# Kernel optimization log

Measured on AMD Instinct MI355X. Metric: run time of the kernel, lower is better.

Reference implementation:

```python
import jax, jax.numpy as jnp
import numpy as np

N_NODES = 50000
N_EDGES = 800000
N_GRAPHS = 512
F_IN = 9
U = 64  # model_units


def _add_self_loops(edge_index, n):
    loop = jnp.arange(n, dtype=edge_index.dtype)
    return jnp.concatenate([edge_index, jnp.stack([loop, loop])], axis=1)


def gat_conv(x, edge_index, W, a_src, a_dst, b):
    # PyG GATConv, heads=1, negative_slope=0.2, add_self_loops=True
    n = x.shape[0]
    ei = _add_self_loops(edge_index, n)
    src, dst = ei[0], ei[1]
    h = x @ W                              # [n, U]
    alpha_s = h @ a_src                    # [n]
    alpha_d = h @ a_dst                    # [n]
    e = jax.nn.leaky_relu(alpha_s[src] + alpha_d[dst], 0.2)   # [E+n]
    m = jax.ops.segment_max(e, dst, num_segments=n)           # stable softmax over incoming edges
    ex = jnp.exp(e - m[dst])
    denom = jax.ops.segment_sum(ex, dst, num_segments=n)
    coef = ex / denom[dst]                 # [E+n]
    out = jax.ops.segment_sum(h[src] * coef[:, None], dst, num_segments=n)
    return out + b


def gcn_conv(x, edge_index, W, b):
    # PyG GCNConv with symmetric normalization and self loops
    n = x.shape[0]
    ei = _add_self_loops(edge_index, n)
    src, dst = ei[0], ei[1]
    h = x @ W                              # [n, U]
    deg = jax.ops.segment_sum(jnp.ones(src.shape, h.dtype), dst, num_segments=n)
    dinv = jnp.where(deg > 0, jax.lax.rsqrt(deg), 0.0)
    norm = dinv[src] * dinv[dst]           # [E+n]
    out = jax.ops.segment_sum(h[src] * norm[:, None], dst, num_segments=n)
    return out + b


def _branch(x, edge_index, W_gat, a_src, a_dst, b_gat, W_gcn, b_gcn, W1, b1, W2, b2, W3, b3):
    x = jnp.tanh(gat_conv(x, edge_index, W_gat, a_src, a_dst, b_gat))
    for i in range(W_gcn.shape[0]):        # model_layers - 1 = 2 GCN layers
        x = jnp.tanh(gcn_conv(x, edge_index, W_gcn[i], b_gcn[i]))
        # dropout is a no-op in eval mode
    x = jnp.tanh(x @ W1 + b1)
    x = jnp.tanh(x @ W2 + b2)
    x = x @ W3 + b3                        # [n, 1]; dropout no-op in eval
    return x


def _mean_pool(x, batch, num_graphs):
    sums = jax.ops.segment_sum(x, batch, num_segments=num_graphs)
    cnt = jax.ops.segment_sum(jnp.ones((x.shape[0],), x.dtype), batch, num_segments=num_graphs)
    return sums / jnp.maximum(cnt, 1.0)[:, None]


def setup_inputs() -> dict:
    key = jax.random.key(0)
    ks = jax.random.split(key, 16)
    inp = {
        "x_a": jax.random.normal(ks[0], (N_NODES, F_IN), jnp.float32),
        "x_b": jax.random.normal(ks[1], (N_NODES, F_IN), jnp.float32),
        "edge_index_a": jax.random.randint(ks[2], (2, N_EDGES), 0, N_NODES, jnp.int32),
        "edge_index_b": jax.random.randint(ks[3], (2, N_EDGES), 0, N_NODES, jnp.int32),
        "batch_a": jnp.sort(jax.random.randint(ks[4], (N_NODES,), 0, N_GRAPHS, jnp.int32)),
        "batch_b": jnp.sort(jax.random.randint(ks[5], (N_NODES,), 0, N_GRAPHS, jnp.int32)),
        # parameters
        "W_gat": jax.random.normal(ks[6], (F_IN, U), jnp.float32) * 0.3,
        "a_src": jax.random.normal(ks[7], (U,), jnp.float32) * 0.3,
        "a_dst": jax.random.normal(ks[8], (U,), jnp.float32) * 0.3,
        "b_gat": jnp.zeros((U,), jnp.float32),
        "W_gcn": jax.random.normal(ks[9], (2, U, U), jnp.float32) * (1.0 / np.sqrt(U)),
        "b_gcn": jnp.zeros((2, U), jnp.float32),
        "W1": jax.random.normal(ks[10], (U, U), jnp.float32) * (1.0 / np.sqrt(U)),
        "b1": jnp.zeros((U,), jnp.float32),
        "W2": jax.random.normal(ks[11], (U, 32), jnp.float32) * (1.0 / np.sqrt(U)),
        "b2": jnp.zeros((32,), jnp.float32),
        "W3": jax.random.normal(ks[12], (32, 1), jnp.float32) * (1.0 / np.sqrt(32.0)),
        "b3": jnp.zeros((1,), jnp.float32),
    }
    return inp


def reference(x_a, x_b, edge_index_a, edge_index_b, batch_a, batch_b,
              W_gat, a_src, a_dst, b_gat, W_gcn, b_gcn, W1, b1, W2, b2, W3, b3):
    params = (W_gat, a_src, a_dst, b_gat, W_gcn, b_gcn, W1, b1, W2, b2, W3, b3)
    ha = _branch(x_a, edge_index_a, *params)
    hb = _branch(x_b, edge_index_b, *params)
    ua = _mean_pool(ha, batch_a, N_GRAPHS)   # [G, 1]
    ub = _mean_pool(hb, batch_b, N_GRAPHS)
    return jax.nn.sigmoid(ub - ua)
```

## Files before the change

### kernel.cpp

```cpp
#include <hip/hip_runtime.h>
#include <hip/hip_fp16.h>
#include <math.h>

#define NN 50000
#define NE 800000
#define NG 512
#define NET (NE + NN)
#define NT2 ((2 * NN + 63) / 64)
#define GN4 ((2 * NN + 3) / 4)
#define GN8 ((2 * NN + 7) / 8)
#define GN32 ((2 * NN + 31) / 32)
#define TS 72

#define SLICE 512
#define NSL ((NN + SLICE - 1) / SLICE)
#define CHK 4096
#define NCK ((NET + CHK - 1) / CHK)
#define CAP 10240

typedef unsigned short u16;
typedef _Float16 h8 __attribute__((ext_vector_type(8)));
typedef float f32x4 __attribute__((ext_vector_type(4)));

__device__ __forceinline__ float wsum64(float v) {
#pragma unroll
    for (int o = 32; o > 0; o >>= 1) v += __shfl_down(v, o, 64);
    return v;
}

__device__ __forceinline__ float fast_tanh(float x) {
    return 1.f - 2.f / (__expf(2.f * x) + 1.f);
}


__global__ __launch_bounds__(256) void k_hist(const int* __restrict__ eia,
                                              const int* __restrict__ eib,
                                              int* __restrict__ cnts) {
    __shared__ int h[NSL];
    int b = blockIdx.x;
    int br = b >= NCK, c = b - (br ? NCK : 0);
    int t = threadIdx.x;
    for (int i = t; i < NSL; i += 256) h[i] = 0;
    __syncthreads();
    const int* ei = br ? eib : eia;
    int e0 = c * CHK, e1 = e0 + CHK; if (e1 > NET) e1 = NET;
    for (int e = e0 + t; e < e1; e += 256) {
        int d = (e < NE) ? __builtin_nontemporal_load(&ei[NE + e]) : (e - NE);
        atomicAdd(&h[d >> 9], 1);
    }
    __syncthreads();
    for (int i = t; i < NSL; i += 256) cnts[(br * NSL + i) * NCK + c] = h[i];
}

__global__ __launch_bounds__(64) void k_off1(int* __restrict__ cnts,
                                             int* __restrict__ sliceBase) {
    int b = blockIdx.x;
    int br = b >= NSL, s = b - (br ? NSL : 0);
    int lane = threadIdx.x;
    int* row = cnts + (br * NSL + s) * NCK;
    int run = 0;
    for (int c0 = 0; c0 < NCK; c0 += 64) {
        int c = c0 + lane;
        int v = (c < NCK) ? row[c] : 0;
        int orig = v;
#pragma unroll
        for (int o = 1; o < 64; o <<= 1) {
            int tv = __shfl_up(v, o, 64);
            if (lane >= o) v += tv;
        }
        if (c < NCK) row[c] = run + v - orig;
        run += __shfl(v, 63, 64);
    }
    if (lane == 0) sliceBase[br * (NSL + 1) + s] = run;
}

__global__ void k_off2(int* __restrict__ sliceBase, int* __restrict__ rowptr2,
                       float* __restrict__ pool) {
    int t = threadIdx.x;
    for (int i = t; i < 4 * NG; i += 256) pool[i] = 0.f;
    if (t < 2) {
        int* sb = sliceBase + t * (NSL + 1);
        int run = 0;
        for (int s = 0; s < NSL; s++) { int v = sb[s]; sb[s] = run; run += v; }
        sb[NSL] = run;
        rowptr2[t * (NN + 1) + NN] = run;
    }
}

__global__ __launch_bounds__(256) void k_bucket(const int* __restrict__ eia,
                                                const int* __restrict__ eib,
                                                const int* __restrict__ cnts,
                                                const int* __restrict__ sliceBase,
                                                unsigned int* __restrict__ staging) {
    __shared__ int cur[NSL];
    int b = blockIdx.x;
    int br = b >= NCK, c = b - (br ? NCK : 0);
    int t = threadIdx.x;
    for (int i = t; i < NSL; i += 256)
        cur[i] = cnts[(br * NSL + i) * NCK + c] + sliceBase[br * (NSL + 1) + i];
    __syncthreads();
    const int* ei = br ? eib : eia;
    unsigned int* stg = staging + (size_t)br * NET;
    int e0 = c * CHK, e1 = e0 + CHK; if (e1 > NET) e1 = NET;
    for (int e = e0 + t; e < e1; e += 256) {
        int d, s;
        if (e < NE) {
            d = __builtin_nontemporal_load(&ei[NE + e]);
            s = __builtin_nontemporal_load(&ei[e]);
        } else { d = e - NE; s = d; }
        int pos = atomicAdd(&cur[d >> 9], 1);
        stg[pos] = ((unsigned int)(d & 511) << 16) | (unsigned int)s;
    }
}

__global__ __launch_bounds__(512) void k_slice(const unsigned int* __restrict__ staging,
                                               const int* __restrict__ sliceBase,
                                               int* __restrict__ rowptr2,
                                               float* __restrict__ dinv2,
                                               u16* __restrict__ csr2) {
    __shared__ int sc[512];
    __shared__ int cur[512];
    __shared__ u16 buf[CAP];
    int b = blockIdx.x;
    int br = b >= NSL, sl = b - (br ? NSL : 0);
    int t = threadIdx.x;
    const int* sb = sliceBase + br * (NSL + 1);
    int base = sb[sl], m = sb[sl + 1] - base;
    const unsigned int* st = staging + (size_t)br * NET + base;
    cur[t] = 0;
    __syncthreads();
    for (int i = t; i < m; i += 512) atomicAdd(&cur[st[i] >> 16], 1);
    __syncthreads();
    int v = cur[t];
    sc[t] = v;
    __syncthreads();
    for (int o = 1; o < 512; o <<= 1) {
        int add = (t >= o) ? sc[t - o] : 0;
        __syncthreads();
        sc[t] += add;
        __syncthreads();
    }
    int excl = sc[t] - v;
    int node = sl * SLICE + t;
    if (node < NN) {
        rowptr2[br * (NN + 1) + node] = base + excl;
        dinv2[br * NN + node] = v > 0 ? rsqrtf((float)v) : 0.f;
    }
    cur[t] = excl;
    __syncthreads();
    for (int i = t; i < m; i += 512) {
        unsigned int e = st[i];
        int pos = atomicAdd(&cur[e >> 16], 1);
        if (pos < CAP) buf[pos] = (u16)(e & 0xffffu);
    }
    __syncthreads();
    u16* out = csr2 + (size_t)br * NET + base;
    int mm = m < CAP ? m : CAP;
    for (int i = t; i < mm; i += 512) out[i] = buf[i];
}

__global__ __launch_bounds__(256) void k_wprep(const float* __restrict__ W1,
                                               const float* __restrict__ W2,
                                               const float* __restrict__ Wgcn,
                                               __half* __restrict__ out) {
    int i = blockIdx.x * 256 + threadIdx.x;
    float v;
    if (i < 4096)       { int n = i >> 6,        k = i & 63; v = W1[k * 64 + n]; }
    else if (i < 6144)  { int j = i - 4096; int n = j >> 6, k = j & 63; v = W2[k * 32 + n]; }
    else if (i < 10240) { int j = i - 6144; int n = j >> 6, k = j & 63; v = Wgcn[k * 64 + n]; }
    else                { int j = i - 10240; int n = j >> 6, k = j & 63; v = Wgcn[4096 + k * 64 + n]; }
    out[i] = __float2half(v);
}


__global__ void k_gat_input(const float* __restrict__ xa, const float* __restrict__ xb,
                            const float* __restrict__ Wg,
                            const float* __restrict__ avs, const float* __restrict__ avd,
                            __half* __restrict__ A, float* __restrict__ als,
                            float* __restrict__ ald) {
    __shared__ float sW[9 * 64];
    __shared__ float sas[64], sad[64];
    int t = threadIdx.x;
    for (int i = t; i < 9 * 64; i += 256) sW[i] = Wg[i];
    if (t < 64) { sas[t] = avs[t]; sad[t] = avd[t]; }
    __syncthreads();
    int n = blockIdx.x * 4 + (t >> 6);
    int u = t & 63;
    if (n >= 2 * NN) return;
    const float* xp = (n < NN) ? &xa[(size_t)n * 9] : &xb[(size_t)(n - NN) * 9];
    float h = 0.f;
#pragma unroll
    for (int f = 0; f < 9; f++) h += xp[f] * sW[f * 64 + u];
    A[(size_t)n * 64 + u] = __float2half(h);
    float ps = wsum64(h * sas[u]);
    float pd = wsum64(h * sad[u]);
    if (u == 0) { als[n] = ps; ald[n] = pd; }
}

__global__ __launch_bounds__(256) void k_edgew(
        const int* __restrict__ rowptr2, const u16* __restrict__ csr2,
        const float* __restrict__ als, const float* __restrict__ ald,
        float* __restrict__ wn) {
    int u = threadIdx.x & 63;
    int lu = u & 31;
    int dg = blockIdx.x * 8 + (threadIdx.x >> 6) * 2 + (u >> 5);
    if (dg >= 2 * NN) return;
    int br = dg >= NN;
    int d = dg - br * NN;
    const int* rp = rowptr2 + br * (NN + 1);
    const u16* cs = csr2 + br * NET;
    float* wp = wn + (size_t)br * NET;
    int nb = br * NN;
    int beg = rp[d], end = rp[d + 1];
    float ad = ald[dg];
    float den = 0.f;
    for (int c = beg + lu; c < end; c += 32) {
        int s = nb + cs[c];
        float v = als[s] + ad;
        float w = __expf(fmaxf(v, 0.2f * v));
        den += w;
        wp[c] = w;
    }
#pragma unroll
    for (int o = 16; o > 0; o >>= 1) den += __shfl_down(den, o, 32);
    den = __shfl(den, 0, 32);
    float inv = 1.f / den;
    for (int c = beg + lu; c < end; c += 32) wp[c] *= inv;
}

__device__ __forceinline__ void fma8(float* acc, float4 f, float w) {
    const __half2* h = (const __half2*)&f;
#pragma unroll
    for (int p = 0; p < 4; p++) {
        float2 v = __half22float2(h[p]);
        acc[2 * p]     += v.x * w;
        acc[2 * p + 1] += v.y * w;
    }
}

__global__ __launch_bounds__(256) void k_gat_gather8(
        const int* __restrict__ rowptr2, const u16* __restrict__ csr2,
        const float* __restrict__ wn, const __half* __restrict__ A,
        const float* __restrict__ bias, __half* __restrict__ B) {
    int lane = threadIdx.x & 63;
    int grp = lane >> 3, li = lane & 7;
    int dg = blockIdx.x * 32 + (threadIdx.x >> 6) * 8 + grp;
    int br = dg >= NN;
    int d = dg - br * NN;
    const int* rp = rowptr2 + br * (NN + 1);
    const u16* cs = csr2 + br * NET;
    const float* wp = wn + (size_t)br * NET;
    int nb = br * NN;
    int beg = rp[d], end = rp[d + 1];
    const float4* Af = (const float4*)A;
    float acc[8];
#pragma unroll
    for (int k = 0; k < 8; k++) acc[k] = 0.f;
    for (int j = beg; j < end; j += 4) {
        int i0 = j, i1 = j + 1, i2 = j + 2, i3 = j + 3;
        int c1 = i1 < end ? i1 : end - 1;
        int c2 = i2 < end ? i2 : end - 1;
        int c3 = i3 < end ? i3 : end - 1;
        float w0 = wp[i0];
        float w1 = i1 < end ? wp[c1] : 0.f;
        float w2 = i2 < end ? wp[c2] : 0.f;
        float w3 = i3 < end ? wp[c3] : 0.f;
        int s0 = nb + cs[i0];
        int s1 = nb + cs[c1];
        int s2 = nb + cs[c2];
        int s3 = nb + cs[c3];
        float4 f0 = Af[(size_t)s0 * 8 + li];
        float4 f1 = Af[(size_t)s1 * 8 + li];
        float4 f2 = Af[(size_t)s2 * 8 + li];
        float4 f3 = Af[(size_t)s3 * 8 + li];
        fma8(acc, f0, w0);
        fma8(acc, f1, w1);
        fma8(acc, f2, w2);
        fma8(acc, f3, w3);
    }
    const float4* bf = (const float4*)bias;
    float4 b0 = bf[2 * li], b1 = bf[2 * li + 1];
    __half2 o[4];
    o[0] = __floats2half2_rn(fast_tanh(acc[0] + b0.x), fast_tanh(acc[1] + b0.y));
    o[1] = __floats2half2_rn(fast_tanh(acc[2] + b0.z), fast_tanh(acc[3] + b0.w));
    o[2] = __floats2half2_rn(fast_tanh(acc[4] + b1.x), fast_tanh(acc[5] + b1.y));
    o[3] = __floats2half2_rn(fast_tanh(acc[6] + b1.z), fast_tanh(acc[7] + b1.w));
    ((float4*)B)[(size_t)dg * 8 + li] = *(float4*)o;
}

__global__ __launch_bounds__(256) void k_gcn_gather8(
        const int* __restrict__ rowptr2, const u16* __restrict__ csr2,
        const float* __restrict__ dinv, const __half* __restrict__ Y,
        const float* __restrict__ bias, __half* __restrict__ Bout) {
    int lane = threadIdx.x & 63;
    int grp = lane >> 3, li = lane & 7;
    int dg = blockIdx.x * 32 + (threadIdx.x >> 6) * 8 + grp;
    int br = dg >= NN;
    int d = dg - br * NN;
    const int* rp = rowptr2 + br * (NN + 1);
    const u16* cs = csr2 + br * NET;
    int nb = br * NN;
    int beg = rp[d], end = rp[d + 1];
    const float4* Yf = (const float4*)Y;
    float acc[8];
#pragma unroll
    for (int k = 0; k < 8; k++) acc[k] = 0.f;
    for (int j = beg; j < end; j += 4) {
        int i1 = j + 1, i2 = j + 2, i3 = j + 3;
        int c1 = i1 < end ? i1 : end - 1;
        int c2 = i2 < end ? i2 : end - 1;
        int c3 = i3 < end ? i3 : end - 1;
        float w1 = i1 < end ? 1.f : 0.f;
        float w2 = i2 < end ? 1.f : 0.f;
        float w3 = i3 < end ? 1.f : 0.f;
        int s0 = nb + cs[j];
        int s1 = nb + cs[c1];
        int s2 = nb + cs[c2];
        int s3 = nb + cs[c3];
        float4 f0 = Yf[(size_t)s0 * 8 + li];
        float4 f1 = Yf[(size_t)s1 * 8 + li];
        float4 f2 = Yf[(size_t)s2 * 8 + li];
        float4 f3 = Yf[(size_t)s3 * 8 + li];
        fma8(acc, f0, 1.f);
        fma8(acc, f1, w1);
        fma8(acc, f2, w2);
        fma8(acc, f3, w3);
    }
    float dv = dinv[dg];
    const float4* bf = (const float4*)bias;
    float4 b0 = bf[2 * li], b1 = bf[2 * li + 1];
    __half2 o[4];
    o[0] = __floats2half2_rn(fast_tanh(acc[0] * dv + b0.x), fast_tanh(acc[1] * dv + b0.y));
    o[1] = __floats2half2_rn(fast_tanh(acc[2] * dv + b0.z), fast_tanh(acc[3] * dv + b0.w));
    o[2] = __floats2half2_rn(fast_tanh(acc[4] * dv + b1.x), fast_tanh(acc[5] * dv + b1.y));
    o[3] = __floats2half2_rn(fast_tanh(acc[6] * dv + b1.z), fast_tanh(acc[7] * dv + b1.w));
    ((float4*)Bout)[(size_t)dg * 8 + li] = *(float4*)o;
}

__global__ __launch_bounds__(256) void k_lin_tile(
        const __half* __restrict__ X, const __half* __restrict__ Wt,
        const float* __restrict__ dinv, __half* __restrict__ Y) {
    __shared__ __half sX[64 * TS];
    __shared__ __half sW[64 * TS];
    int t = threadIdx.x;
    int base = blockIdx.x * 64;
    const float4* Xf = (const float4*)X;
    const float4* Wf = (const float4*)Wt;
#pragma unroll
    for (int rep = 0; rep < 2; rep++) {
        int i = t + rep * 256;
        int row = i >> 3, q = i & 7;
        *(float4*)&sW[row * TS + q * 8] = Wf[i];
        float4 x;
        if (base + row < 2 * NN) x = Xf[(size_t)(base + row) * 8 + q];
        else x = make_float4(0.f, 0.f, 0.f, 0.f);
        *(float4*)&sX[row * TS + q * 8] = x;
    }
    __syncthreads();
    int l = t & 63, w = t >> 6;
    int lr = l & 15, lg = l >> 4;
    h8 av0 = *(const h8*)&sX[(16 * w + lr) * TS + 8 * lg];
    h8 av1 = *(const h8*)&sX[(16 * w + lr) * TS + 32 + 8 * lg];
    f32x4 acc[4];
#pragma unroll
    for (int s = 0; s < 4; s++) {
        h8 bv0 = *(const h8*)&sW[(16 * s + lr) * TS + 8 * lg];
        h8 bv1 = *(const h8*)&sW[(16 * s + lr) * TS + 32 + 8 * lg];
        f32x4 c = {0.f, 0.f, 0.f, 0.f};
        c = __builtin_amdgcn_mfma_f32_16x16x32_f16(av0, bv0, c, 0, 0, 0);
        c = __builtin_amdgcn_mfma_f32_16x16x32_f16(av1, bv1, c, 0, 0, 0);
        acc[s] = c;
    }
    int nrow = base + 16 * w + 4 * lg;
    float4 dv4 = *(const float4*)&dinv[16 * w + 4 * lg + base];
#pragma unroll
    for (int s = 0; s < 4; s++) {
        int col = 16 * s + lr;
#pragma unroll
        for (int i = 0; i < 4; i++) {
            int n = nrow + i;
            if (n < 2 * NN) Y[(size_t)n * 64 + col] = __float2half(acc[s][i] * dv4[i]);
        }
    }
}

__global__ __launch_bounds__(256) void k_mlp_pool(
        const __half* __restrict__ X,
        const int* __restrict__ batch_a, const int* __restrict__ batch_b,
        const __half* __restrict__ W1t, const float* __restrict__ b1,
        const __half* __restrict__ W2t, const float* __restrict__ b2,
        const float* __restrict__ W3, const float* __restrict__ b3,
        float* __restrict__ pool) {
    __shared__ __half sX[64 * TS];
    __shared__ __half sW1[64 * TS];
    __shared__ __half sW2[32 * TS];
    __shared__ float sP[64];
    __shared__ int sKey[64];
    __shared__ float sVal[64];
    int t = threadIdx.x;
    int base = blockIdx.x * 64;
    const float4* Xf = (const float4*)X;
    const float4* W1f = (const float4*)W1t;
    const float4* W2f = (const float4*)W2t;
#pragma unroll
    for (int rep = 0; rep < 2; rep++) {
        int i = t + rep * 256;
        int row = i >> 3, q = i & 7;
        *(float4*)&sW1[row * TS + q * 8] = W1f[i];
        float4 x;
        if (base + row < 2 * NN) x = Xf[(size_t)(base + row) * 8 + q];
        else x = make_float4(0.f, 0.f, 0.f, 0.f);
        *(float4*)&sX[row * TS + q * 8] = x;
    }
    {
        int row = t >> 3, q = t & 7;
        *(float4*)&sW2[row * TS + q * 8] = W2f[t];
    }
    float bb3 = b3[0];
    __syncthreads();
    int l = t & 63, w = t >> 6;
    int lr = l & 15, lg = l >> 4;
    h8 av0 = *(const h8*)&sX[(16 * w + lr) * TS + 8 * lg];
    h8 av1 = *(const h8*)&sX[(16 * w + lr) * TS + 32 + 8 * lg];
    f32x4 d1[4];
#pragma unroll
    for (int s = 0; s < 4; s++) {
        float bias = b1[16 * s + lr];
        f32x4 c = {bias, bias, bias, bias};
        h8 bv0 = *(const h8*)&sW1[(16 * s + lr) * TS + 8 * lg];
        h8 bv1 = *(const h8*)&sW1[(16 * s + lr) * TS + 32 + 8 * lg];
        c = __builtin_amdgcn_mfma_f32_16x16x32_f16(av0, bv0, c, 0, 0, 0);
        c = __builtin_amdgcn_mfma_f32_16x16x32_f16(av1, bv1, c, 0, 0, 0);
        d1[s] = c;
    }
#pragma unroll
    for (int s = 0; s < 4; s++) {
#pragma unroll
        for (int i = 0; i < 4; i++) {
            sX[(16 * w + 4 * lg + i) * TS + 16 * s + lr] = __float2half(fast_tanh(d1[s][i]));
        }
    }
    __syncthreads();
    h8 a20 = *(const h8*)&sX[(16 * w + lr) * TS + 8 * lg];
    h8 a21 = *(const h8*)&sX[(16 * w + lr) * TS + 32 + 8 * lg];
    f32x4 d2[2];
#pragma unroll
    for (int s = 0; s < 2; s++) {
        float bias = b2[16 * s + lr];
        f32x4 c = {bias, bias, bias, bias};
        h8 bv0 = *(const h8*)&sW2[(16 * s + lr) * TS + 8 * lg];
        h8 bv1 = *(const h8*)&sW2[(16 * s + lr) * TS + 32 + 8 * lg];
        c = __builtin_amdgcn_mfma_f32_16x16x32_f16(a20, bv0, c, 0, 0, 0);
        c = __builtin_amdgcn_mfma_f32_16x16x32_f16(a21, bv1, c, 0, 0, 0);
        d2[s] = c;
    }
    float w3a = W3[lr], w3b = W3[16 + lr];
    float pr[4];
#pragma unroll
    for (int i = 0; i < 4; i++)
        pr[i] = fast_tanh(d2[0][i]) * w3a + fast_tanh(d2[1][i]) * w3b;
#pragma unroll
    for (int o = 1; o < 16; o <<= 1) {
#pragma unroll
        for (int i = 0; i < 4; i++) pr[i] += __shfl_xor(pr[i], o, 16);
    }
    if (lr == 0) {
#pragma unroll
        for (int i = 0; i < 4; i++) sP[16 * w + 4 * lg + i] = pr[i];
    }
    __syncthreads();
    if (t < 64) {
        int n = base + t;
        bool valid = n < 2 * NN;
        int br = n >= NN;
        int g = valid ? (br ? batch_b[n - NN] : batch_a[n]) : -1;
        int key = valid ? (br * 4096 + g) : -1;
        sKey[t] = key;
        sVal[t] = sP[t] + bb3;
        __builtin_amdgcn_s_barrier();
        if (valid && (t == 0 || sKey[t - 1] != key)) {
            float sum = 0.f;
            int cnt = 0;
            for (int j = t; j < 64 && sKey[j] == key; j++) { sum += sVal[j]; cnt++; }
            float* bin = pool + br * 2 * NG;
            atomicAdd(&bin[g], sum);
            atomicAdd(&bin[NG + g], (float)cnt);
        }
    }
}

__global__ void k_final(const float* __restrict__ pool, float* __restrict__ out) {
    int g = blockIdx.x * 256 + threadIdx.x;
    if (g >= NG) return;
    float ua = pool[g] / fmaxf(pool[NG + g], 1.f);
    float ub = pool[2 * NG + g] / fmaxf(pool[3 * NG + g], 1.f);
    float z = ub - ua;
    out[g] = 1.f / (1.f + __expf(-z));
}

extern "C" void kernel_launch(void* const* d_in, const int* in_sizes, int n_in,
                              void* d_out, int out_size, void* d_ws, size_t ws_size,
                              hipStream_t stream) {
    const float* x_a = (const float*)d_in[0];
    const float* x_b = (const float*)d_in[1];
    const int* ei_a = (const int*)d_in[2];
    const int* ei_b = (const int*)d_in[3];
    const int* batch_a = (const int*)d_in[4];
    const int* batch_b = (const int*)d_in[5];
    const float* Wg   = (const float*)d_in[6];
    const float* avs  = (const float*)d_in[7];
    const float* avd  = (const float*)d_in[8];
    const float* bg   = (const float*)d_in[9];
    const float* Wgcn = (const float*)d_in[10];
    const float* bgcn = (const float*)d_in[11];
    const float* W1 = (const float*)d_in[12];
    const float* b1 = (const float*)d_in[13];
    const float* W2 = (const float*)d_in[14];
    const float* b2 = (const float*)d_in[15];
    const float* W3 = (const float*)d_in[16];
    const float* b3 = (const float*)d_in[17];

    char* w = (char*)d_ws;
    __half* A2 = (__half*)w;          w += (size_t)2 * NN * 64 * 2;
    __half* B2 = (__half*)w;          w += (size_t)2 * NN * 64 * 2;
    float* als2 = (float*)w;          w += (size_t)2 * NN * 4;
    float* ald2 = (float*)w;          w += (size_t)2 * NN * 4;
    float* dinv2 = (float*)w;         w += (size_t)2 * NN * 4;
    float* pool = (float*)w;          w += (size_t)4 * NG * 4;
    int* rowptr2 = (int*)w;           w += (size_t)2 * (NN + 1) * 4;
    int* cnts = (int*)w;              w += (size_t)2 * NSL * NCK * 4;
    int* sliceBase = (int*)w;         w += (size_t)2 * (NSL + 1) * 4;
    u16* csr2 = (u16*)w;              w += (size_t)2 * NET * 2;
    float* wn = (float*)w;            w += (size_t)2 * NET * 4;
    __half* wcache = (__half*)w;      w += (size_t)14336 * 2;
    unsigned int* staging = (unsigned int*)A2;

    __half* W1t = wcache;
    __half* W2t = wcache + 4096;
    __half* Wg0t = wcache + 6144;
    __half* Wg1t = wcache + 10240;

    dim3 blk(256);

    k_hist<<<2 * NCK, blk, 0, stream>>>(ei_a, ei_b, cnts);
    k_wprep<<<56, blk, 0, stream>>>(W1, W2, Wgcn, wcache);
    k_off1<<<2 * NSL, dim3(64), 0, stream>>>(cnts, sliceBase);
    k_off2<<<1, blk, 0, stream>>>(sliceBase, rowptr2, pool);
    k_bucket<<<2 * NCK, blk, 0, stream>>>(ei_a, ei_b, cnts, sliceBase, staging);
    k_slice<<<2 * NSL, dim3(512), 0, stream>>>(staging, sliceBase, rowptr2, dinv2, csr2);

    k_gat_input<<<GN4, blk, 0, stream>>>(x_a, x_b, Wg, avs, avd, A2, als2, ald2);
    k_edgew<<<GN8, blk, 0, stream>>>(rowptr2, csr2, als2, ald2, wn);
    k_gat_gather8<<<GN32, blk, 0, stream>>>(rowptr2, csr2, wn, A2, bg, B2);
    k_lin_tile<<<NT2, blk, 0, stream>>>(B2, Wg0t, dinv2, A2);
    k_gcn_gather8<<<GN32, blk, 0, stream>>>(rowptr2, csr2, dinv2, A2, bgcn, B2);
    k_lin_tile<<<NT2, blk, 0, stream>>>(B2, Wg1t, dinv2, A2);
    k_gcn_gather8<<<GN32, blk, 0, stream>>>(rowptr2, csr2, dinv2, A2, bgcn + 64, B2);
    k_mlp_pool<<<NT2, blk, 0, stream>>>(B2, batch_a, batch_b, W1t, b1, W2t, b2, W3, b3, pool);

    k_final<<<(NG + 255) / 256, blk, 0, stream>>>(pool, (float*)d_out);
}
```

Measured before the change: 304.4 us.

## Split node features into 32-wide halves and fuse GAT edge weights into gather

Node feature buffers move from row-major [n,64] fp16 to two planes of [n,32], and the gather kernels process one half per block. Block IDs are interleaved so paired half-blocks run close together. The goal is a smaller random-access working set per gather pass, which should improve L2 hit rates. The separate edge-weight kernel and its wn buffer are removed: GAT weights are recomputed inside the gather, with normalization applied at the end. The cost is that exp is computed twice, once for each half, and the CSR indices are read twice.

Result: no change. 304.9 us (+0.2%).

```diff
diff --git a/kernel.cpp b/kernel.cpp
--- a/kernel.cpp
+++ b/kernel.cpp
@@ -8,9 +8,10 @@
 #define NET (NE + NN)
 #define NT2 ((2 * NN + 63) / 64)
 #define GN4 ((2 * NN + 3) / 4)
-#define GN8 ((2 * NN + 7) / 8)
-#define GN32 ((2 * NN + 31) / 32)
 #define TS 72
+#define HOFF ((size_t)2 * NN * 32)
+#define GXB 391
+#define GX (8 * GXB)
 
 #define SLICE 512
 #define NSL ((NN + SLICE - 1) / SLICE)
@@ -191,41 +192,10 @@
     float h = 0.f;
 #pragma unroll
     for (int f = 0; f < 9; f++) h += xp[f] * sW[f * 64 + u];
-    A[(size_t)n * 64 + u] = __float2half(h);
+    A[(size_t)(u >> 5) * HOFF + (size_t)n * 32 + (u & 31)] = __float2half(h);
     float ps = wsum64(h * sas[u]);
     float pd = wsum64(h * sad[u]);
     if (u == 0) { als[n] = ps; ald[n] = pd; }
-}
-
-__global__ __launch_bounds__(256) void k_edgew(
-        const int* __restrict__ rowptr2, const u16* __restrict__ csr2,
-        const float* __restrict__ als, const float* __restrict__ ald,
-        float* __restrict__ wn) {
-    int u = threadIdx.x & 63;
-    int lu = u & 31;
-    int dg = blockIdx.x * 8 + (threadIdx.x >> 6) * 2 + (u >> 5);
-    if (dg >= 2 * NN) return;
-    int br = dg >= NN;
-    int d = dg - br * NN;
-    const int* rp = rowptr2 + br * (NN + 1);
-    const u16* cs = csr2 + br * NET;
-    float* wp = wn + (size_t)br * NET;
-    int nb = br * NN;
-    int beg = rp[d], end = rp[d + 1];
-    float ad = ald[dg];
-    float den = 0.f;
-    for (int c = beg + lu; c < end; c += 32) {
-        int s = nb + cs[c];
-        float v = als[s] + ad;
-        float w = __expf(fmaxf(v, 0.2f * v));
-        den += w;
-        wp[c] = w;
-    }
-#pragma unroll
-    for (int o = 16; o > 0; o >>= 1) den += __shfl_down(den, o, 32);
-    den = __shfl(den, 0, 32);
-    float inv = 1.f / den;
-    for (int c = beg + lu; c < end; c += 32) wp[c] *= inv;
 }
 
 __device__ __forceinline__ void fma8(float* acc, float4 f, float w) {
@@ -238,73 +208,91 @@
     }
 }
 
-__global__ __launch_bounds__(256) void k_gat_gather8(
+__global__ __launch_bounds__(256) void k_gat_gather(
         const int* __restrict__ rowptr2, const u16* __restrict__ csr2,
-        const float* __restrict__ wn, const __half* __restrict__ A,
-        const float* __restrict__ bias, __half* __restrict__ B) {
-    int lane = threadIdx.x & 63;
-    int grp = lane >> 3, li = lane & 7;
-    int dg = blockIdx.x * 32 + (threadIdx.x >> 6) * 8 + grp;
-    int br = dg >= NN;
-    int d = dg - br * NN;
+        const float* __restrict__ als, const float* __restrict__ ald,
+        const __half* __restrict__ A, const float* __restrict__ bias,
+        __half* __restrict__ B) {
+    int bid = blockIdx.x;
+    int br = (bid >> 2) & 1;
+    int h = (bid >> 1) & 1;
+    int k = ((bid >> 3) << 1) + (bid & 1);
+    int t = threadIdx.x;
+    int lane = t & 63;
+    int grp = lane >> 2, li = lane & 3;
+    int d = k * 64 + ((t >> 6) << 4) + grp;
+    if (d >= NN) return;
+    int dg = br * NN + d;
     const int* rp = rowptr2 + br * (NN + 1);
     const u16* cs = csr2 + br * NET;
-    const float* wp = wn + (size_t)br * NET;
     int nb = br * NN;
     int beg = rp[d], end = rp[d + 1];
-    const float4* Af = (const float4*)A;
+    float ad = ald[dg];
+    const float4* Af = (const float4*)A + (size_t)h * 2 * NN * 4;
     float acc[8];
 #pragma unroll
-    for (int k = 0; k < 8; k++) acc[k] = 0.f;
+    for (int q = 0; q < 8; q++) acc[q] = 0.f;
+    float den = 0.f;
     for (int j = beg; j < end; j += 4) {
-        int i0 = j, i1 = j + 1, i2 = j + 2, i3 = j + 3;
+        int i1 = j + 1, i2 = j + 2, i3 = j + 3;
         int c1 = i1 < end ? i1 : end - 1;
         int c2 = i2 < end ? i2 : end - 1;
         int c3 = i3 < end ? i3 : end - 1;
-        float w0 = wp[i0];
-        float w1 = i1 < end ? wp[c1] : 0.f;
-        float w2 = i2 < end ? wp[c2] : 0.f;
-        float w3 = i3 < end ? wp[c3] : 0.f;
-        int s0 = nb + cs[i0];
+        int s0 = nb + cs[j];
         int s1 = nb + cs[c1];
         int s2 = nb + cs[c2];
         int s3 = nb + cs[c3];
-        float4 f0 = Af[(size_t)s0 * 8 + li];
-        float4 f1 = Af[(size_t)s1 * 8 + li];
-        float4 f2 = Af[(size_t)s2 * 8 + li];
-        float4 f3 = Af[(size_t)s3 * 8 + li];
+        float v0 = als[s0] + ad;
+        float v1 = als[s1] + ad;
+        float v2 = als[s2] + ad;
+        float v3 = als[s3] + ad;
+        float w0 = __expf(fmaxf(v0, 0.2f * v0));
+        float w1 = i1 < end ? __expf(fmaxf(v1, 0.2f * v1)) : 0.f;
+        float w2 = i2 < end ? __expf(fmaxf(v2, 0.2f * v2)) : 0.f;
+        float w3 = i3 < end ? __expf(fmaxf(v3, 0.2f * v3)) : 0.f;
+        den += (w0 + w1) + (w2 + w3);
+        float4 f0 = Af[(size_t)s0 * 4 + li];
+        float4 f1 = Af[(size_t)s1 * 4 + li];
+        float4 f2 = Af[(size_t)s2 * 4 + li];
+        float4 f3 = Af[(size_t)s3 * 4 + li];
         fma8(acc, f0, w0);
         fma8(acc, f1, w1);
         fma8(acc, f2, w2);
         fma8(acc, f3, w3);
     }
+    float inv = 1.f / den;
     const float4* bf = (const float4*)bias;
-    float4 b0 = bf[2 * li], b1 = bf[2 * li + 1];
+    float4 b0 = bf[h * 8 + li * 2], b1 = bf[h * 8 + li * 2 + 1];
     __half2 o[4];
-    o[0] = __floats2half2_rn(fast_tanh(acc[0] + b0.x), fast_tanh(acc[1] + b0.y));
-    o[1] = __floats2half2_rn(fast_tanh(acc[2] + b0.z), fast_tanh(acc[3] + b0.w));
-    o[2] = __floats2half2_rn(fast_tanh(acc[4] + b1.x), fast_tanh(acc[5] + b1.y));
-    o[3] = __floats2half2_rn(fast_tanh(acc[6] + b1.z), fast_tanh(acc[7] + b1.w));
-    ((float4*)B)[(size_t)dg * 8 + li] = *(float4*)o;
-}
-
-__global__ __launch_bounds__(256) void k_gcn_gather8(
+    o[0] = __floats2half2_rn(fast_tanh(acc[0] * inv + b0.x), fast_tanh(acc[1] * inv + b0.y));
+    o[1] = __floats2half2_rn(fast_tanh(acc[2] * inv + b0.z), fast_tanh(acc[3] * inv + b0.w));
+    o[2] = __floats2half2_rn(fast_tanh(acc[4] * inv + b1.x), fast_tanh(acc[5] * inv + b1.y));
+    o[3] = __floats2half2_rn(fast_tanh(acc[6] * inv + b1.z), fast_tanh(acc[7] * inv + b1.w));
+    ((float4*)B)[(size_t)h * 2 * NN * 4 + (size_t)dg * 4 + li] = *(float4*)o;
+}
+
+__global__ __launch_bounds__(256) void k_gcn_gather(
         const int* __restrict__ rowptr2, const u16* __restrict__ csr2,
         const float* __restrict__ dinv, const __half* __restrict__ Y,
         const float* __restrict__ bias, __half* __restrict__ Bout) {
-    int lane = threadIdx.x & 63;
-    int grp = lane >> 3, li = lane & 7;
-    int dg = blockIdx.x * 32 + (threadIdx.x >> 6) * 8 + grp;
-    int br = dg >= NN;
-    int d = dg - br * NN;
+    int bid = blockIdx.x;
+    int br = (bid >> 2) & 1;
+    int h = (bid >> 1) & 1;
+    int k = ((bid >> 3) << 1) + (bid & 1);
+    int t = threadIdx.x;
+    int lane = t & 63;
+    int grp = lane >> 2, li = lane & 3;
+    int d = k * 64 + ((t >> 6) << 4) + grp;
+    if (d >= NN) return;
+    int dg = br * NN + d;
     const int* rp = rowptr2 + br * (NN + 1);
     const u16* cs = csr2 + br * NET;
     int nb = br * NN;
     int beg = rp[d], end = rp[d + 1];
-    const float4* Yf = (const float4*)Y;
+    const float4* Yf = (const float4*)Y + (size_t)h * 2 * NN * 4;
     float acc[8];
 #pragma unroll
-    for (int k = 0; k < 8; k++) acc[k] = 0.f;
+    for (int q = 0; q < 8; q++) acc[q] = 0.f;
     for (int j = beg; j < end; j += 4) {
         int i1 = j + 1, i2 = j + 2, i3 = j + 3;
         int c1 = i1 < end ? i1 : end - 1;
@@ -317,10 +305,10 @@
         int s1 = nb + cs[c1];
         int s2 = nb + cs[c2];
         int s3 = nb + cs[c3];
-        float4 f0 = Yf[(size_t)s0 * 8 + li];
-        float4 f1 = Yf[(size_t)s1 * 8 + li];
-        float4 f2 = Yf[(size_t)s2 * 8 + li];
-        float4 f3 = Yf[(size_t)s3 * 8 + li];
+        float4 f0 = Yf[(size_t)s0 * 4 + li];
+        float4 f1 = Yf[(size_t)s1 * 4 + li];
+        float4 f2 = Yf[(size_t)s2 * 4 + li];
+        float4 f3 = Yf[(size_t)s3 * 4 + li];
         fma8(acc, f0, 1.f);
         fma8(acc, f1, w1);
         fma8(acc, f2, w2);
@@ -328,13 +316,28 @@
     }
     float dv = dinv[dg];
     const float4* bf = (const float4*)bias;
-    float4 b0 = bf[2 * li], b1 = bf[2 * li + 1];
+    float4 b0 = bf[h * 8 + li * 2], b1 = bf[h * 8 + li * 2 + 1];
     __half2 o[4];
     o[0] = __floats2half2_rn(fast_tanh(acc[0] * dv + b0.x), fast_tanh(acc[1] * dv + b0.y));
     o[1] = __floats2half2_rn(fast_tanh(acc[2] * dv + b0.z), fast_tanh(acc[3] * dv + b0.w));
     o[2] = __floats2half2_rn(fast_tanh(acc[4] * dv + b1.x), fast_tanh(acc[5] * dv + b1.y));
     o[3] = __floats2half2_rn(fast_tanh(acc[6] * dv + b1.z), fast_tanh(acc[7] * dv + b1.w));
-    ((float4*)Bout)[(size_t)dg * 8 + li] = *(float4*)o;
+    ((float4*)Bout)[(size_t)h * 2 * NN * 4 + (size_t)dg * 4 + li] = *(float4*)o;
+}
+
+__device__ __forceinline__ void stage_split(const __half* __restrict__ X, int base,
+                                            __half* sX, int t) {
+    const float4* Xf = (const float4*)X;
+#pragma unroll
+    for (int rep = 0; rep < 2; rep++) {
+        int i = t + rep * 256;
+        int row = i >> 3, q = i & 7;
+        int h = q >> 2, q2 = q & 3;
+        float4 x;
+        if (base + row < 2 * NN) x = Xf[(size_t)h * 2 * NN * 4 + (size_t)(base + row) * 4 + q2];
+        else x = make_float4(0.f, 0.f, 0.f, 0.f);
+        *(float4*)&sX[row * TS + q * 8] = x;
+    }
 }
 
 __global__ __launch_bounds__(256) void k_lin_tile(
@@ -344,18 +347,14 @@
     __shared__ __half sW[64 * TS];
     int t = threadIdx.x;
     int base = blockIdx.x * 64;
-    const float4* Xf = (const float4*)X;
     const float4* Wf = (const float4*)Wt;
 #pragma unroll
     for (int rep = 0; rep < 2; rep++) {
         int i = t + rep * 256;
         int row = i >> 3, q = i & 7;
         *(float4*)&sW[row * TS + q * 8] = Wf[i];
-        float4 x;
-        if (base + row < 2 * NN) x = Xf[(size_t)(base + row) * 8 + q];
-        else x = make_float4(0.f, 0.f, 0.f, 0.f);
-        *(float4*)&sX[row * TS + q * 8] = x;
-    }
+    }
+    stage_split(X, base, sX, t);
     __syncthreads();
     int l = t & 63, w = t >> 6;
     int lr = l & 15, lg = l >> 4;
@@ -376,10 +375,11 @@
 #pragma unroll
     for (int s = 0; s < 4; s++) {
         int col = 16 * s + lr;
+        size_t cbase = (size_t)(col >> 5) * HOFF + (col & 31);
 #pragma unroll
         for (int i = 0; i < 4; i++) {
             int n = nrow + i;
-            if (n < 2 * NN) Y[(size_t)n * 64 + col] = __float2half(acc[s][i] * dv4[i]);
+            if (n < 2 * NN) Y[cbase + (size_t)n * 32] = __float2half(acc[s][i] * dv4[i]);
         }
     }
 }
@@ -399,7 +399,6 @@
     __shared__ float sVal[64];
     int t = threadIdx.x;
     int base = blockIdx.x * 64;
-    const float4* Xf = (const float4*)X;
     const float4* W1f = (const float4*)W1t;
     const float4* W2f = (const float4*)W2t;
 #pragma unroll
@@ -407,15 +406,12 @@
         int i = t + rep * 256;
         int row = i >> 3, q = i & 7;
         *(float4*)&sW1[row * TS + q * 8] = W1f[i];
-        float4 x;
-        if (base + row < 2 * NN) x = Xf[(size_t)(base + row) * 8 + q];
-        else x = make_float4(0.f, 0.f, 0.f, 0.f);
-        *(float4*)&sX[row * TS + q * 8] = x;
     }
     {
         int row = t >> 3, q = t & 7;
         *(float4*)&sW2[row * TS + q * 8] = W2f[t];
     }
+    stage_split(X, base, sX, t);
     float bb3 = b3[0];
     __syncthreads();
     int l = t & 63, w = t >> 6;
@@ -531,7 +527,6 @@
     int* cnts = (int*)w;              w += (size_t)2 * NSL * NCK * 4;
     int* sliceBase = (int*)w;         w += (size_t)2 * (NSL + 1) * 4;
     u16* csr2 = (u16*)w;              w += (size_t)2 * NET * 2;
-    float* wn = (float*)w;            w += (size_t)2 * NET * 4;
     __half* wcache = (__half*)w;      w += (size_t)14336 * 2;
     unsigned int* staging = (unsigned int*)A2;
 
@@ -550,12 +545,11 @@
     k_slice<<<2 * NSL, dim3(512), 0, stream>>>(staging, sliceBase, rowptr2, dinv2, csr2);
 
     k_gat_input<<<GN4, blk, 0, stream>>>(x_a, x_b, Wg, avs, avd, A2, als2, ald2);
-    k_edgew<<<GN8, blk, 0, stream>>>(rowptr2, csr2, als2, ald2, wn);
-    k_gat_gather8<<<GN32, blk, 0, stream>>>(rowptr2, csr2, wn, A2, bg, B2);
+    k_gat_gather<<<GX, blk, 0, stream>>>(rowptr2, csr2, als2, ald2, A2, bg, B2);
     k_lin_tile<<<NT2, blk, 0, stream>>>(B2, Wg0t, dinv2, A2);
-    k_gcn_gather8<<<GN32, blk, 0, stream>>>(rowptr2, csr2, dinv2, A2, bgcn, B2);
+    k_gcn_gather<<<GX, blk, 0, stream>>>(rowptr2, csr2, dinv2, A2, bgcn, B2);
     k_lin_tile<<<NT2, blk, 0, stream>>>(B2, Wg1t, dinv2, A2);
-    k_gcn_gather8<<<GN32, blk, 0, stream>>>(rowptr2, csr2, dinv2, A2, bgcn + 64, B2);
+    k_gcn_gather<<<GX, blk, 0, stream>>>(rowptr2, csr2, dinv2, A2, bgcn + 64, B2);
     k_mlp_pool<<<NT2, blk, 0, stream>>>(B2, batch_a, batch_b, W1t, b1, W2t, b2, W3, b3, pool);
 
     k_final<<<(NG + 255) / 256, blk, 0, stream>>>(pool, (float*)d_out);
```

## Fuse GAT edge-weight softmax into gather kernel and widen gather unroll to 8

Applied to the files above, without the earlier changes.

Removes the separate edge-weight kernel. Each gather group now computes the unnormalized exp attention weights inline from als/ald and keeps a running denominator, scaling by its inverse at the end. This avoids writing and re-reading a weight array the size of the edge list plus one launch. In exchange, every lane in a group recomputes the exp redundantly. Both GAT and GCN gathers now unroll 8 edges per iteration instead of 4 to keep more loads in flight, at the cost of more registers and more wasted work on the padded tail.

Result: slower. 316.3 us (+3.9%).

```diff
diff --git a/kernel.cpp b/kernel.cpp
--- a/kernel.cpp
+++ b/kernel.cpp
@@ -8,7 +8,6 @@
 #define NET (NE + NN)
 #define NT2 ((2 * NN + 63) / 64)
 #define GN4 ((2 * NN + 3) / 4)
-#define GN8 ((2 * NN + 7) / 8)
 #define GN32 ((2 * NN + 31) / 32)
 #define TS 72
 
@@ -197,94 +196,66 @@
     if (u == 0) { als[n] = ps; ald[n] = pd; }
 }
 
-__global__ __launch_bounds__(256) void k_edgew(
+__device__ __forceinline__ void fma8(float* acc, float4 f, float w) {
+    const __half2* h = (const __half2*)&f;
+#pragma unroll
+    for (int p = 0; p < 4; p++) {
+        float2 v = __half22float2(h[p]);
+        acc[2 * p]     += v.x * w;
+        acc[2 * p + 1] += v.y * w;
+    }
+}
+
+__global__ __launch_bounds__(256) void k_gat_gather8(
         const int* __restrict__ rowptr2, const u16* __restrict__ csr2,
         const float* __restrict__ als, const float* __restrict__ ald,
-        float* __restrict__ wn) {
-    int u = threadIdx.x & 63;
-    int lu = u & 31;
-    int dg = blockIdx.x * 8 + (threadIdx.x >> 6) * 2 + (u >> 5);
-    if (dg >= 2 * NN) return;
+        const __half* __restrict__ A, const float* __restrict__ bias,
+        __half* __restrict__ B) {
+    int lane = threadIdx.x & 63;
+    int grp = lane >> 3, li = lane & 7;
+    int dg = blockIdx.x * 32 + ((threadIdx.x >> 6) << 3) + grp;
     int br = dg >= NN;
     int d = dg - br * NN;
     const int* rp = rowptr2 + br * (NN + 1);
     const u16* cs = csr2 + br * NET;
-    float* wp = wn + (size_t)br * NET;
     int nb = br * NN;
     int beg = rp[d], end = rp[d + 1];
     float ad = ald[dg];
-    float den = 0.f;
-    for (int c = beg + lu; c < end; c += 32) {
-        int s = nb + cs[c];
-        float v = als[s] + ad;
-        float w = __expf(fmaxf(v, 0.2f * v));
-        den += w;
-        wp[c] = w;
-    }
-#pragma unroll
-    for (int o = 16; o > 0; o >>= 1) den += __shfl_down(den, o, 32);
-    den = __shfl(den, 0, 32);
-    float inv = 1.f / den;
-    for (int c = beg + lu; c < end; c += 32) wp[c] *= inv;
-}
-
-__device__ __forceinline__ void fma8(float* acc, float4 f, float w) {
-    const __half2* h = (const __half2*)&f;
-#pragma unroll
-    for (int p = 0; p < 4; p++) {
-        float2 v = __half22float2(h[p]);
-        acc[2 * p]     += v.x * w;
-        acc[2 * p + 1] += v.y * w;
-    }
-}
-
-__global__ __launch_bounds__(256) void k_gat_gather8(
-        const int* __restrict__ rowptr2, const u16* __restrict__ csr2,
-        const float* __restrict__ wn, const __half* __restrict__ A,
-        const float* __restrict__ bias, __half* __restrict__ B) {
-    int lane = threadIdx.x & 63;
-    int grp = lane >> 3, li = lane & 7;
-    int dg = blockIdx.x * 32 + (threadIdx.x >> 6) * 8 + grp;
-    int br = dg >= NN;
-    int d = dg - br * NN;
-    const int* rp = rowptr2 + br * (NN + 1);
-    const u16* cs = csr2 + br * NET;
-    const float* wp = wn + (size_t)br * NET;
-    int nb = br * NN;
-    int beg = rp[d], end = rp[d + 1];
     const float4* Af = (const float4*)A;
     float acc[8];
 #pragma unroll
-    for (int k = 0; k < 8; k++) acc[k] = 0.f;
-    for (int j = beg; j < end; j += 4) {
-        int i0 = j, i1 = j + 1, i2 = j + 2, i3 = j + 3;
-        int c1 = i1 < end ? i1 : end - 1;
-        int c2 = i2 < end ? i2 : end - 1;
-        int c3 = i3 < end ? i3 : end - 1;
-        float w0 = wp[i0];
-        float w1 = i1 < end ? wp[c1] : 0.f;
-        float w2 = i2 < end ? wp[c2] : 0.f;
-        float w3 = i3 < end ? wp[c3] : 0.f;
-        int s0 = nb + cs[i0];
-        int s1 = nb + cs[c1];
-        int s2 = nb + cs[c2];
-        int s3 = nb + cs[c3];
-        float4 f0 = Af[(size_t)s0 * 8 + li];
-        float4 f1 = Af[(size_t)s1 * 8 + li];
-        float4 f2 = Af[(size_t)s2 * 8 + li];
-        float4 f3 = Af[(size_t)s3 * 8 + li];
-        fma8(acc, f0, w0);
-        fma8(acc, f1, w1);
-        fma8(acc, f2, w2);
-        fma8(acc, f3, w3);
-    }
+    for (int q = 0; q < 8; q++) acc[q] = 0.f;
+    float den = 0.f;
+    for (int j = beg; j < end; j += 8) {
+        int sv[8];
+        float wv[8];
+#pragma unroll
+        for (int e = 0; e < 8; e++) {
+            int c_ = (j + e < end) ? j + e : end - 1;
+            sv[e] = nb + cs[c_];
+        }
+#pragma unroll
+        for (int e = 0; e < 8; e++) {
+            float v = als[sv[e]] + ad;
+            float w = __expf(fmaxf(v, 0.2f * v));
+            wv[e] = (j + e < end) ? w : 0.f;
+        }
+#pragma unroll
+        for (int e = 0; e < 8; e++) den += wv[e];
+        float4 fv[8];
+#pragma unroll
+        for (int e = 0; e < 8; e++) fv[e] = Af[(size_t)sv[e] * 8 + li];
+#pragma unroll
+        for (int e = 0; e < 8; e++) fma8(acc, fv[e], wv[e]);
+    }
+    float inv = 1.f / den;
     const float4* bf = (const float4*)bias;
     float4 b0 = bf[2 * li], b1 = bf[2 * li + 1];
     __half2 o[4];
-    o[0] = __floats2half2_rn(fast_tanh(acc[0] + b0.x), fast_tanh(acc[1] + b0.y));
-    o[1] = __floats2half2_rn(fast_tanh(acc[2] + b0.z), fast_tanh(acc[3] + b0.w));
-    o[2] = __floats2half2_rn(fast_tanh(acc[4] + b1.x), fast_tanh(acc[5] + b1.y));
-    o[3] = __floats2half2_rn(fast_tanh(acc[6] + b1.z), fast_tanh(acc[7] + b1.w));
+    o[0] = __floats2half2_rn(fast_tanh(acc[0] * inv + b0.x), fast_tanh(acc[1] * inv + b0.y));
+    o[1] = __floats2half2_rn(fast_tanh(acc[2] * inv + b0.z), fast_tanh(acc[3] * inv + b0.w));
+    o[2] = __floats2half2_rn(fast_tanh(acc[4] * inv + b1.x), fast_tanh(acc[5] * inv + b1.y));
+    o[3] = __floats2half2_rn(fast_tanh(acc[6] * inv + b1.z), fast_tanh(acc[7] * inv + b1.w));
     ((float4*)B)[(size_t)dg * 8 + li] = *(float4*)o;
 }
 
@@ -294,7 +265,7 @@
         const float* __restrict__ bias, __half* __restrict__ Bout) {
     int lane = threadIdx.x & 63;
     int grp = lane >> 3, li = lane & 7;
-    int dg = blockIdx.x * 32 + (threadIdx.x >> 6) * 8 + grp;
+    int dg = blockIdx.x * 32 + ((threadIdx.x >> 6) << 3) + grp;
     int br = dg >= NN;
     int d = dg - br * NN;
     const int* rp = rowptr2 + br * (NN + 1);
@@ -304,27 +275,21 @@
     const float4* Yf = (const float4*)Y;
     float acc[8];
 #pragma unroll
-    for (int k = 0; k < 8; k++) acc[k] = 0.f;
-    for (int j = beg; j < end; j += 4) {
-        int i1 = j + 1, i2 = j + 2, i3 = j + 3;
-        int c1 = i1 < end ? i1 : end - 1;
-        int c2 = i2 < end ? i2 : end - 1;
-        int c3 = i3 < end ? i3 : end - 1;
-        float w1 = i1 < end ? 1.f : 0.f;
-        float w2 = i2 < end ? 1.f : 0.f;
-        float w3 = i3 < end ? 1.f : 0.f;
-        int s0 = nb + cs[j];
-        int s1 = nb + cs[c1];
-        int s2 = nb + cs[c2];
-        int s3 = nb + cs[c3];
-        float4 f0 = Yf[(size_t)s0 * 8 + li];
-        float4 f1 = Yf[(size_t)s1 * 8 + li];
-        float4 f2 = Yf[(size_t)s2 * 8 + li];
-        float4 f3 = Yf[(size_t)s3 * 8 + li];
-        fma8(acc, f0, 1.f);
-        fma8(acc, f1, w1);
-        fma8(acc, f2, w2);
-        fma8(acc, f3, w3);
+    for (int q = 0; q < 8; q++) acc[q] = 0.f;
+    for (int j = beg; j < end; j += 8) {
+        int sv[8];
+        float wv[8];
+#pragma unroll
+        for (int e = 0; e < 8; e++) {
+            int c_ = (j + e < end) ? j + e : end - 1;
+            sv[e] = nb + cs[c_];
+            wv[e] = (j + e < end) ? 1.f : 0.f;
+        }
+        float4 fv[8];
+#pragma unroll
+        for (int e = 0; e < 8; e++) fv[e] = Yf[(size_t)sv[e] * 8 + li];
+#pragma unroll
+        for (int e = 0; e < 8; e++) fma8(acc, fv[e], wv[e]);
     }
     float dv = dinv[dg];
     const float4* bf = (const float4*)bias;
@@ -531,7 +496,6 @@
     int* cnts = (int*)w;              w += (size_t)2 * NSL * NCK * 4;
     int* sliceBase = (int*)w;         w += (size_t)2 * (NSL + 1) * 4;
     u16* csr2 = (u16*)w;              w += (size_t)2 * NET * 2;
-    float* wn = (float*)w;            w += (size_t)2 * NET * 4;
     __half* wcache = (__half*)w;      w += (size_t)14336 * 2;
     unsigned int* staging = (unsigned int*)A2;
 
@@ -550,8 +514,7 @@
     k_slice<<<2 * NSL, dim3(512), 0, stream>>>(staging, sliceBase, rowptr2, dinv2, csr2);
 
     k_gat_input<<<GN4, blk, 0, stream>>>(x_a, x_b, Wg, avs, avd, A2, als2, ald2);
-    k_edgew<<<GN8, blk, 0, stream>>>(rowptr2, csr2, als2, ald2, wn);
-    k_gat_gather8<<<GN32, blk, 0, stream>>>(rowptr2, csr2, wn, A2, bg, B2);
+    k_gat_gather8<<<GN32, blk, 0, stream>>>(rowptr2, csr2, als2, ald2, A2, bg, B2);
     k_lin_tile<<<NT2, blk, 0, stream>>>(B2, Wg0t, dinv2, A2);
     k_gcn_gather8<<<GN32, blk, 0, stream>>>(rowptr2, csr2, dinv2, A2, bgcn, B2);
     k_lin_tile<<<NT2, blk, 0, stream>>>(B2, Wg1t, dinv2, A2);
```
